# Kernel tuning notes

Hardware: AMD Instinct MI355X
Metric: run time of the kernel (lower is better)

Reference implementation:

```python
import jax, jax.numpy as jnp
import numpy as np
from jax import lax

BEV_SIZE = 250
BEV_RANGE = 50.0
BEV_RES = 0.4
SZ = BEV_SIZE * BEV_SIZE
N_POINTS = 5_000_000
EPS = 1e-5


def setup_inputs() -> dict:
    key = jax.random.key(0)
    ks = jax.random.split(key, 8)
    # points: x,y in [-55,55) (some out of range), z in [-3,5), intensity in [0,1)
    xy = jax.random.uniform(ks[0], (N_POINTS, 2), jnp.float32, -55.0, 55.0)
    z = jax.random.uniform(ks[1], (N_POINTS, 1), jnp.float32, -3.0, 5.0)
    it = jax.random.uniform(ks[2], (N_POINTS, 1), jnp.float32, 0.0, 1.0)
    points = jnp.concatenate([xy, z, it], axis=1)

    def he(k, shape):
        fan_in = shape[1] * shape[2] * shape[3]
        return jax.random.normal(k, shape, jnp.float32) * np.sqrt(2.0 / fan_in)

    return {
        "points": points,
        "w1": he(ks[3], (32, 4, 3, 3)), "b1": jnp.zeros(32), "g1": jnp.ones(32), "beta1": jnp.zeros(32),
        "w2": he(ks[4], (64, 32, 3, 3)), "b2": jnp.zeros(64), "g2": jnp.ones(64), "beta2": jnp.zeros(64),
        "w3": he(ks[5], (64, 64, 3, 3)), "b3": jnp.zeros(64), "g3": jnp.ones(64), "beta3": jnp.zeros(64),
    }


def points_to_bev(points):
    x, y, z, inten = points[:, 0], points[:, 1], points[:, 2], points[:, 3]
    valid = (x >= -BEV_RANGE) & (x < BEV_RANGE) & (y >= -BEV_RANGE) & (y < BEV_RANGE)
    xi = jnp.clip(((x + BEV_RANGE) / BEV_RES).astype(jnp.int32), 0, BEV_SIZE - 1)
    yi = jnp.clip(((y + BEV_RANGE) / BEV_RES).astype(jnp.int32), 0, BEV_SIZE - 1)
    # invalid points routed to an extra dummy bin SZ, sliced off afterwards
    flat = jnp.where(valid, yi * BEV_SIZE + xi, SZ)

    max_z = jnp.full(SZ + 1, -jnp.inf, jnp.float32).at[flat].max(z)[:SZ]
    max_z = jnp.where(jnp.isinf(max_z), 0.0, max_z)
    min_z = jnp.full(SZ + 1, jnp.inf, jnp.float32).at[flat].min(z)[:SZ]
    min_z = jnp.where(jnp.isinf(min_z), 0.0, min_z)
    density = jnp.zeros(SZ + 1, jnp.float32).at[flat].add(1.0)[:SZ]
    isum = jnp.zeros(SZ + 1, jnp.float32).at[flat].add(inten)[:SZ]
    mean_i = jnp.where(density > 0, isum / jnp.maximum(density, 1.0), 0.0)

    bev = jnp.stack([max_z, min_z, jnp.log1p(density), mean_i], axis=0)
    return bev.reshape(4, BEV_SIZE, BEV_SIZE)


def conv_bn_relu(x, w, b, g, beta):
    # x: (1, Cin, H, W), w: (Cout, Cin, 3, 3)
    y = lax.conv_general_dilated(x, w, (1, 1), "SAME",
                                 dimension_numbers=("NCHW", "OIHW", "NCHW"))
    y = y + b[None, :, None, None]
    # BatchNorm2d in training mode: batch stats over (N, H, W)
    mu = jnp.mean(y, axis=(0, 2, 3), keepdims=True)
    var = jnp.mean((y - mu) ** 2, axis=(0, 2, 3), keepdims=True)
    y = (y - mu) * lax.rsqrt(var + EPS)
    y = y * g[None, :, None, None] + beta[None, :, None, None]
    return jax.nn.relu(y)


def reference(points, w1, b1, g1, beta1, w2, b2, g2, beta2, w3, b3, g3, beta3):
    bev = points_to_bev(points)[None]  # (1, 4, 250, 250)
    h = conv_bn_relu(bev, w1, b1, g1, beta1)
    h = conv_bn_relu(h, w2, b2, g2, beta2)
    h = conv_bn_relu(h, w3, b3, g3, beta3)
    return h  # (1, 64, 250, 250)
```

## Files before the change

kernel.cpp:

```cpp
#include <hip/hip_runtime.h>


constexpr int BEVW = 250;
constexpr int SZC  = BEVW * BEVW;
constexpr int NB   = 512;
constexpr int PPT  = 16;
constexpr int CHUNK = 256 * PPT;
constexpr int NBKT = 100;
constexpr int NCELL = 625;
constexpr int CAPB = 43008;
constexpr int NSL  = 8;
constexpr int NSPL = 4;

__device__ __forceinline__ unsigned f2ord(float f) {
    unsigned u = __float_as_uint(f);
    return (u & 0x80000000u) ? ~u : (u | 0x80000000u);
}
__device__ __forceinline__ float ord2f(unsigned u) {
    unsigned b = (u & 0x80000000u) ? (u & 0x7FFFFFFFu) : ~u;
    return __uint_as_float(b);
}

__global__ void k_prep(const float* __restrict__ w1, float* __restrict__ wt1,
                       const float* __restrict__ w2, float* __restrict__ wt2,
                       const float* __restrict__ w3, float* __restrict__ wt3,
                       unsigned* __restrict__ gcnt) {
    int i = blockIdx.x * blockDim.x + threadIdx.x;
    if (i < 128) gcnt[i] = 0u;
    constexpr int N1 = 32 * 4 * 9;
    constexpr int N2 = 64 * 32 * 9;
    constexpr int N3 = 64 * 64 * 9;
    if (i < N1) {
        int oc = i / 36, r = i % 36, ic = r / 9, k = r % 9;
        wt1[(ic * 9 + k) * 32 + oc] = w1[i];
    } else if (i < N1 + N2) {
        int e = i - N1;
        int oc = e / 288, r = e % 288, ic = r / 9, k = r % 9;
        wt2[(ic * 9 + k) * 64 + oc] = w2[e];
    } else if (i < N1 + N2 + N3) {
        int e = i - N1 - N2;
        int oc = e / 576, r = e % 576, ic = r / 9, k = r % 9;
        wt3[(ic * 9 + k) * 64 + oc] = w3[e];
    }
}

__launch_bounds__(256)
__global__ void k_bucket(const float4* __restrict__ pts, int n,
                         unsigned long long* __restrict__ recs,
                         unsigned* __restrict__ gcnt) {
    __shared__ unsigned lcnt[NBKT];
    __shared__ unsigned lbase[NBKT];
    const int tid = threadIdx.x;
    if (tid < NBKT) lcnt[tid] = 0u;
    __syncthreads();

    const int ppb = (n + NB - 1) / NB;
    const int start = blockIdx.x * ppb;
    const int end = min(start + ppb, n);

    for (int c0 = start; c0 < end; c0 += CHUNK) {
        unsigned long long rec[PPT];
        int bkt[PPT];
        unsigned slot[PPT];
        unsigned vmask = 0u;
#pragma unroll
        for (int k = 0; k < PPT; ++k) {
            int p = c0 + k * 256 + tid;
            if (p >= end) continue;
            float4 q = pts[p];
            if (!(q.x >= -50.0f && q.x < 50.0f && q.y >= -50.0f && q.y < 50.0f))
                continue;
            int xi = (int)((q.x + 50.0f) / 0.4f);
            int yi = (int)((q.y + 50.0f) / 0.4f);
            xi = min(max(xi, 0), BEVW - 1);
            yi = min(max(yi, 0), BEVW - 1);
            int b  = (yi / 25) * 10 + (xi / 25);
            int cl = (yi % 25) * 25 + (xi % 25);
            unsigned iq = (unsigned)(q.w * 4194304.0f);
            rec[k] = ((unsigned long long)f2ord(q.z) << 32) |
                     ((unsigned long long)(unsigned)cl << 22) | iq;
            bkt[k] = b;
            slot[k] = atomicAdd(&lcnt[b], 1u);
            vmask |= 1u << k;
        }
        __syncthreads();
        if (tid < NBKT) {
            unsigned c = lcnt[tid];
            if (c) lbase[tid] = atomicAdd(&gcnt[tid], c);
            lcnt[tid] = 0u;
        }
        __syncthreads();
#pragma unroll
        for (int k = 0; k < PPT; ++k) {
            if (!((vmask >> k) & 1u)) continue;
            unsigned idx = lbase[bkt[k]] + slot[k];
            if (idx < (unsigned)CAPB)
                recs[(size_t)bkt[k] * CAPB + idx] = rec[k];
        }
    }
}

__launch_bounds__(1024)
__global__ void k_reduce(const unsigned long long* __restrict__ recs,
                         const unsigned* __restrict__ gcnt,
                         float* __restrict__ bev) {
    __shared__ unsigned mxA[NCELL], mnA[NCELL], ctA[NCELL], siA[NCELL];
    const int b = blockIdx.x;
    for (int i = threadIdx.x; i < NCELL; i += 1024) {
        mxA[i] = 0u; mnA[i] = 0xFFFFFFFFu; ctA[i] = 0u; siA[i] = 0u;
    }
    __syncthreads();
    const unsigned nb = min(gcnt[b], (unsigned)CAPB);
    const unsigned long long* rb = recs + (size_t)b * CAPB;
    for (unsigned i = threadIdx.x; i < nb; i += 1024) {
        unsigned long long r = rb[i];
        unsigned zo = (unsigned)(r >> 32);
        unsigned cl = ((unsigned)(r >> 22)) & 0x3FFu;
        unsigned iq = (unsigned)r & 0x3FFFFFu;
        atomicMax(&mxA[cl], zo);
        atomicMin(&mnA[cl], zo);
        atomicAdd(&ctA[cl], 1u);
        atomicAdd(&siA[cl], iq);
    }
    __syncthreads();
    const int tx = b % 10, ty = b / 10;
    for (int i = threadIdx.x; i < NCELL; i += 1024) {
        int cy = ty * 25 + i / 25, cx = tx * 25 + i % 25;
        int cell = cy * BEVW + cx;
        unsigned c = ctA[i];
        bool has = c > 0u;
        float dn = (float)c;
        float isum = (float)siA[i] * (1.0f / 4194304.0f);
        bev[0 * SZC + cell] = has ? ord2f(mxA[i]) : 0.0f;
        bev[1 * SZC + cell] = has ? ord2f(mnA[i]) : 0.0f;
        bev[2 * SZC + cell] = log1pf(dn);
        bev[3 * SZC + cell] = has ? isum / dn : 0.0f;
    }
}

__launch_bounds__(1024)
__global__ void k_reduceP(const unsigned long long* __restrict__ recs,
                          const unsigned* __restrict__ gcnt,
                          uint4* __restrict__ parts) {
    __shared__ unsigned mxA[NCELL], mnA[NCELL], ctA[NCELL], siA[NCELL];
    const int b = blockIdx.x, s = blockIdx.y;
    for (int i = threadIdx.x; i < NCELL; i += 1024) {
        mxA[i] = 0u; mnA[i] = 0xFFFFFFFFu; ctA[i] = 0u; siA[i] = 0u;
    }
    __syncthreads();
    const unsigned nb = min(gcnt[b], (unsigned)CAPB);
    const unsigned lo = nb * (unsigned)s / NSPL;
    const unsigned hi = nb * (unsigned)(s + 1) / NSPL;
    const unsigned long long* rb = recs + (size_t)b * CAPB;
    for (unsigned i = lo + threadIdx.x; i < hi; i += 1024) {
        unsigned long long r = rb[i];
        unsigned zo = (unsigned)(r >> 32);
        unsigned cl = ((unsigned)(r >> 22)) & 0x3FFu;
        unsigned iq = (unsigned)r & 0x3FFFFFu;
        atomicMax(&mxA[cl], zo);
        atomicMin(&mnA[cl], zo);
        atomicAdd(&ctA[cl], 1u);
        atomicAdd(&siA[cl], iq);
    }
    __syncthreads();
    uint4* dst = parts + ((size_t)b * NSPL + s) * NCELL;
    for (int i = threadIdx.x; i < NCELL; i += 1024)
        dst[i] = make_uint4(mxA[i], mnA[i], ctA[i], siA[i]);
}

__global__ void k_merge(const uint4* __restrict__ parts, float* __restrict__ bev) {
    int t = blockIdx.x * blockDim.x + threadIdx.x;
    if (t >= NBKT * NCELL) return;
    const int b = t / NCELL, i = t % NCELL;
    unsigned mx = 0u, mn = 0xFFFFFFFFu, ct = 0u, si = 0u;
#pragma unroll
    for (int s = 0; s < NSPL; ++s) {
        uint4 p = parts[((size_t)b * NSPL + s) * NCELL + i];
        mx = max(mx, p.x);
        mn = min(mn, p.y);
        ct += p.z;
        si += p.w;
    }
    const int tx = b % 10, ty = b / 10;
    int cy = ty * 25 + i / 25, cx = tx * 25 + i % 25;
    int cell = cy * BEVW + cx;
    bool has = ct > 0u;
    float dn = (float)ct;
    float isum = (float)si * (1.0f / 4194304.0f);
    bev[0 * SZC + cell] = has ? ord2f(mx) : 0.0f;
    bev[1 * SZC + cell] = has ? ord2f(mn) : 0.0f;
    bev[2 * SZC + cell] = log1pf(dn);
    bev[3 * SZC + cell] = has ? isum / dn : 0.0f;
}

template <int CIN, int COUT, int ICB, int OCG, bool FUSE>
__launch_bounds__(256)
__global__ void k_conv(const float* __restrict__ in, const float* __restrict__ wt,
                       const float* __restrict__ bias,
                       const double* __restrict__ part, const float* __restrict__ g,
                       const float* __restrict__ beta,
                       float* __restrict__ out) {
    constexpr int RS = 24;
    __shared__ float s_in[ICB][18 * RS];
    __shared__ float sAB[2 * CIN];

    const int tid = threadIdx.x;
    const int u = tid & 15, v = tid >> 4;
    const int tile = blockIdx.x;
    const int tx = (tile & 15) * 16, ty = (tile >> 4) * 16;
    const int oc0 = blockIdx.y * OCG;
    const bool interior = (tx >= 16) && (tx <= 224) && (ty >= 16) && (ty <= 224);

    if (FUSE) {
        for (int c = tid; c < CIN; c += 256) {
            double S = 0.0, S2 = 0.0;
            for (int s = 0; s < NSL; ++s) {
                S  += part[(c * NSL + s) * 2];
                S2 += part[(c * NSL + s) * 2 + 1];
            }
            double mu  = S / (double)SZC;
            double var = S2 / (double)SZC - mu * mu;
            double A = (1.0 / sqrt(var + 1e-5)) * (double)g[c];
            sAB[2 * c]     = (float)A;
            sAB[2 * c + 1] = (float)((double)beta[c] - mu * A);
        }
    }

    float acc[OCG];
#pragma unroll
    for (int o = 0; o < OCG; ++o) acc[o] = 0.0f;

    for (int ic0 = 0; ic0 < CIN; ic0 += ICB) {
        __syncthreads();
        if (interior) {
            const float* base = in + (size_t)ic0 * SZC + (ty - 1) * BEVW + (tx - 1);
            for (int e = tid; e < ICB * 144; e += 256) {
                int c = e / 144, rr = e % 144;
                int r = rr >> 3, pp = rr & 7;
                int q = 1 + 2 * pp;
                float2 x2 = *(const float2*)(base + (size_t)c * SZC + r * BEVW + q);
                if (FUSE) {
                    int cg = ic0 + c;
                    float A = sAB[2 * cg], Bc = sAB[2 * cg + 1];
                    x2.x = fmaxf(fmaf(x2.x, A, Bc), 0.0f);
                    x2.y = fmaxf(fmaf(x2.y, A, Bc), 0.0f);
                }
                *(float2*)&s_in[c][r * RS + q + 1] = x2;
            }
            for (int e = tid; e < ICB * 36; e += 256) {
                int c = e / 36, t = e % 36;
                int r = t >> 1, q = (t & 1) ? 17 : 0;
                float x = base[(size_t)c * SZC + r * BEVW + q];
                if (FUSE) {
                    int cg = ic0 + c;
                    x = fmaxf(fmaf(x, sAB[2 * cg], sAB[2 * cg + 1]), 0.0f);
                }
                s_in[c][r * RS + q + 1] = x;
            }
        } else {
            for (int e = tid; e < ICB * 324; e += 256) {
                int c = e / 324, rem = e % 324;
                int r = rem / 18, q = rem % 18;
                int cg = ic0 + c;
                int gy = ty - 1 + r, gx = tx - 1 + q;
                float x = 0.0f;
                if (gy >= 0 && gy < BEVW && gx >= 0 && gx < BEVW) {
                    x = in[(size_t)cg * SZC + gy * BEVW + gx];
                    if (FUSE) x = fmaxf(fmaf(x, sAB[2 * cg], sAB[2 * cg + 1]), 0.0f);
                }
                s_in[c][r * RS + q + 1] = x;
            }
        }
        __syncthreads();

#pragma unroll
        for (int icl = 0; icl < ICB; ++icl) {
            const int icg = ic0 + icl;
#pragma unroll
            for (int tap = 0; tap < 9; ++tap) {
                const int ky = tap / 3, kx = tap % 3;
                float x = s_in[icl][(v + ky) * RS + (u + kx) + 1];
                const float* wk = wt + ((size_t)(icg * 9 + tap) * COUT + oc0);
#pragma unroll
                for (int o = 0; o < OCG; ++o)
                    acc[o] = fmaf(x, wk[o], acc[o]);
            }
        }
    }

    const int ox = tx + u, oy = ty + v;
    if (ox < BEVW && oy < BEVW) {
#pragma unroll
        for (int o = 0; o < OCG; ++o)
            out[(size_t)(oc0 + o) * SZC + oy * BEVW + ox] = acc[o] + bias[oc0 + o];
    }
}

__global__ void k_bnstats1(const float* __restrict__ y, double* __restrict__ part) {
    const int c = blockIdx.x, s = blockIdx.y;
    const int lo = s * ((SZC + NSL - 1) / NSL);
    const int hi = min(lo + (SZC + NSL - 1) / NSL, SZC);
    const float* p = y + (size_t)c * SZC;
    double sm = 0.0, s2 = 0.0;
    for (int i = lo + threadIdx.x; i < hi; i += 256) {
        float v = p[i];
        sm += (double)v;
        s2 += (double)v * (double)v;
    }
    for (int off = 32; off; off >>= 1) {
        sm += __shfl_down(sm, off);
        s2 += __shfl_down(s2, off);
    }
    __shared__ double sh[8];
    int wid = threadIdx.x >> 6;
    if ((threadIdx.x & 63) == 0) { sh[wid * 2] = sm; sh[wid * 2 + 1] = s2; }
    __syncthreads();
    if (threadIdx.x == 0) {
        double S = 0.0, S2 = 0.0;
        for (int wv = 0; wv < 4; ++wv) { S += sh[wv * 2]; S2 += sh[wv * 2 + 1]; }
        part[(c * NSL + s) * 2]     = S;
        part[(c * NSL + s) * 2 + 1] = S2;
    }
}

__global__ void k_bnreluS(const float* __restrict__ y, const double* __restrict__ part,
                          const float* __restrict__ g, const float* __restrict__ beta,
                          float* __restrict__ out) {
    int c = blockIdx.y;
    int i = blockIdx.x * blockDim.x + threadIdx.x;
    if (i >= SZC) return;
    double S = 0.0, S2 = 0.0;
    for (int s = 0; s < NSL; ++s) {
        S  += part[(c * NSL + s) * 2];
        S2 += part[(c * NSL + s) * 2 + 1];
    }
    double mu  = S / (double)SZC;
    double var = S2 / (double)SZC - mu * mu;
    double Ad = (1.0 / sqrt(var + 1e-5)) * (double)g[c];
    float A = (float)Ad;
    float B = (float)((double)beta[c] - mu * Ad);
    size_t idx = (size_t)c * SZC + i;
    out[idx] = fmaxf(fmaf(y[idx], A, B), 0.0f);
}

extern "C" void kernel_launch(void* const* d_in, const int* in_sizes, int n_in,
                              void* d_out, int out_size, void* d_ws, size_t ws_size,
                              hipStream_t stream) {
    const float4* pts = (const float4*)d_in[0];
    const float* w1 = (const float*)d_in[1];
    const float* b1 = (const float*)d_in[2];
    const float* g1 = (const float*)d_in[3];
    const float* be1 = (const float*)d_in[4];
    const float* w2 = (const float*)d_in[5];
    const float* b2 = (const float*)d_in[6];
    const float* g2 = (const float*)d_in[7];
    const float* be2 = (const float*)d_in[8];
    const float* w3 = (const float*)d_in[9];
    const float* b3 = (const float*)d_in[10];
    const float* g3 = (const float*)d_in[11];
    const float* be3 = (const float*)d_in[12];

    float* ws = (float*)d_ws;
    const size_t wsf = ws_size / 4;

    constexpr size_t TAILF = 128 + 250000 + 64 + 128 + 128 + 2048 + 1152 + 18432 + 36864;
    float* tail = ws + (wsf - TAILF);
    unsigned* gcnt = (unsigned*)tail;
    float* bev = tail + 128;
    float* st1 = bev + 4 * SZC;
    float* st2 = st1 + 64;
    float* st3 = st2 + 128;
    double* part = (double*)(st3 + 128);
    float* wt1 = st3 + 128 + 2048;
    float* wt2 = wt1 + 1152;
    float* wt3 = wt2 + 18432;
    (void)st1; (void)st2; (void)st3;

    unsigned long long* recs = (unsigned long long*)ws;
    constexpr size_t RECS_F = (size_t)NBKT * CAPB * 2;
    float* y1 = ws;
    float* y2 = ws + 2000000;
    float* out = (float*)d_out;

    constexpr size_t PARTS_F = (size_t)NBKT * NSPL * NCELL * 4;
    const bool splitR = wsf >= RECS_F + PARTS_F + TAILF + 1024;
    uint4* partsR = (uint4*)(ws + RECS_F);

    int n = in_sizes[0] / 4;
    const int cellBlocks = (SZC + 255) / 256;

    k_prep<<<(56448 + 255) / 256, 256, 0, stream>>>(w1, wt1, w2, wt2, w3, wt3, gcnt);

    k_bucket<<<NB, 256, 0, stream>>>(pts, n, recs, gcnt);
    if (splitR) {
        k_reduceP<<<dim3(NBKT, NSPL), 1024, 0, stream>>>(recs, gcnt, partsR);
        k_merge<<<(NBKT * NCELL + 255) / 256, 256, 0, stream>>>(partsR, bev);
    } else {
        k_reduce<<<NBKT, 1024, 0, stream>>>(recs, gcnt, bev);
    }

    k_conv<4, 32, 4, 16, false><<<dim3(256, 2), 256, 0, stream>>>(
        bev, wt1, b1, nullptr, nullptr, nullptr, y1);
    k_bnstats1<<<dim3(32, NSL), 256, 0, stream>>>(y1, part);

    k_conv<32, 64, 8, 16, true><<<dim3(256, 4), 256, 0, stream>>>(
        y1, wt2, b2, part, g1, be1, y2);
    k_bnstats1<<<dim3(64, NSL), 256, 0, stream>>>(y2, part);

    k_conv<64, 64, 8, 16, true><<<dim3(256, 4), 256, 0, stream>>>(
        y2, wt3, b3, part, g2, be2, out);
    k_bnstats1<<<dim3(64, NSL), 256, 0, stream>>>(out, part);

    k_bnreluS<<<dim3(cellBlocks, 64), 256, 0, stream>>>(out, part, g3, be3, out);
}
```

Before: 277.1 us.

## Use 16x16 power-of-two BEV buckets instead of 25x25 tiles

```diff
diff --git a/kernel.cpp b/kernel.cpp
--- a/kernel.cpp
+++ b/kernel.cpp
@@ -6,11 +6,11 @@
 constexpr int NB   = 512;
 constexpr int PPT  = 16;
 constexpr int CHUNK = 256 * PPT;
-constexpr int NBKT = 100;
-constexpr int NCELL = 625;
-constexpr int CAPB = 43008;
+constexpr int NBKT = 256;
+constexpr int NCELL = 256;
+constexpr int CAPB = 18432;
 constexpr int NSL  = 8;
-constexpr int NSPL = 4;
+constexpr int NSPL = 2;
 
 __device__ __forceinline__ unsigned f2ord(float f) {
     unsigned u = __float_as_uint(f);
@@ -26,7 +26,7 @@
                        const float* __restrict__ w3, float* __restrict__ wt3,
                        unsigned* __restrict__ gcnt) {
     int i = blockIdx.x * blockDim.x + threadIdx.x;
-    if (i < 128) gcnt[i] = 0u;
+    if (i < NBKT) gcnt[i] = 0u;
     constexpr int N1 = 32 * 4 * 9;
     constexpr int N2 = 64 * 32 * 9;
     constexpr int N3 = 64 * 64 * 9;
@@ -51,7 +51,7 @@
     __shared__ unsigned lcnt[NBKT];
     __shared__ unsigned lbase[NBKT];
     const int tid = threadIdx.x;
-    if (tid < NBKT) lcnt[tid] = 0u;
+    lcnt[tid] = 0u;
     __syncthreads();
 
     const int ppb = (n + NB - 1) / NB;
@@ -74,8 +74,8 @@
             int yi = (int)((q.y + 50.0f) / 0.4f);
             xi = min(max(xi, 0), BEVW - 1);
             yi = min(max(yi, 0), BEVW - 1);
-            int b  = (yi / 25) * 10 + (xi / 25);
-            int cl = (yi % 25) * 25 + (xi % 25);
+            int b  = (yi & 0xF0) | (xi >> 4);
+            int cl = ((yi & 15) << 4) | (xi & 15);
             unsigned iq = (unsigned)(q.w * 4194304.0f);
             rec[k] = ((unsigned long long)f2ord(q.z) << 32) |
                      ((unsigned long long)(unsigned)cl << 22) | iq;
@@ -84,7 +84,7 @@
             vmask |= 1u << k;
         }
         __syncthreads();
-        if (tid < NBKT) {
+        {
             unsigned c = lcnt[tid];
             if (c) lbase[tid] = atomicAdd(&gcnt[tid], c);
             lcnt[tid] = 0u;
@@ -123,9 +123,10 @@
         atomicAdd(&siA[cl], iq);
     }
     __syncthreads();
-    const int tx = b % 10, ty = b / 10;
+    const int bx = b & 15, by = b >> 4;
     for (int i = threadIdx.x; i < NCELL; i += 1024) {
-        int cy = ty * 25 + i / 25, cx = tx * 25 + i % 25;
+        int cy = by * 16 + (i >> 4), cx = bx * 16 + (i & 15);
+        if (cy >= BEVW || cx >= BEVW) continue;
         int cell = cy * BEVW + cx;
         unsigned c = ctA[i];
         bool has = c > 0u;
@@ -171,7 +172,10 @@
 __global__ void k_merge(const uint4* __restrict__ parts, float* __restrict__ bev) {
     int t = blockIdx.x * blockDim.x + threadIdx.x;
     if (t >= NBKT * NCELL) return;
-    const int b = t / NCELL, i = t % NCELL;
+    const int b = t >> 8, i = t & 255;
+    const int bx = b & 15, by = b >> 4;
+    int cy = by * 16 + (i >> 4), cx = bx * 16 + (i & 15);
+    if (cy >= BEVW || cx >= BEVW) return;
     unsigned mx = 0u, mn = 0xFFFFFFFFu, ct = 0u, si = 0u;
 #pragma unroll
     for (int s = 0; s < NSPL; ++s) {
@@ -181,8 +185,6 @@
         ct += p.z;
         si += p.w;
     }
-    const int tx = b % 10, ty = b / 10;
-    int cy = ty * 25 + i / 25, cx = tx * 25 + i % 25;
     int cell = cy * BEVW + cx;
     bool has = ct > 0u;
     float dn = (float)ct;
@@ -363,18 +365,16 @@
     float* ws = (float*)d_ws;
     const size_t wsf = ws_size / 4;
 
-    constexpr size_t TAILF = 128 + 250000 + 64 + 128 + 128 + 2048 + 1152 + 18432 + 36864;
+    constexpr size_t TAILF = 256 + 250000 + 64 + 128 + 128 + 2048 + 1152 + 18432 + 36864;
     float* tail = ws + (wsf - TAILF);
     unsigned* gcnt = (unsigned*)tail;
-    float* bev = tail + 128;
-    float* st1 = bev + 4 * SZC;
-    float* st2 = st1 + 64;
-    float* st3 = st2 + 128;
-    double* part = (double*)(st3 + 128);
-    float* wt1 = st3 + 128 + 2048;
+    float* bev = tail + 256;
+    float* pad0 = bev + 4 * SZC;
+    double* part = (double*)(pad0 + 320);
+    float* wt1 = pad0 + 320 + 2048;
     float* wt2 = wt1 + 1152;
     float* wt3 = wt2 + 18432;
-    (void)st1; (void)st2; (void)st3;
+    (void)pad0;
 
     unsigned long long* recs = (unsigned long long*)ws;
     constexpr size_t RECS_F = (size_t)NBKT * CAPB * 2;
```

New measurement: 277.0 us. Within noise of the previous version (-0.0%).
